# Kernel tuning notes

Measured on AMD Instinct MI355X. Metric: run time of the kernel, lower is better.

The kernel has to match this reference:

```python
import jax, jax.numpy as jnp
import numpy as np
from jax import lax

B, N, C = 128, 197, 384      # batch, tokens (1 cls + 14*14), embed dim
H, HD = 6, 64                # num_heads, head_dim
HID = 1536                   # mlp hidden = 4*C
S = 14                       # spatial side, S*S = N-1
SCALE = HD ** -0.5


def setup_inputs() -> dict:
    key = jax.random.key(0)
    ks = jax.random.split(key, 12)
    rn = lambda k, shp, s=0.02: jax.random.normal(k, shp, jnp.float32) * s
    return {
        "x": jax.random.normal(ks[0], (B, N, C), jnp.float32),
        "ln1_g": jnp.ones((C,), jnp.float32), "ln1_b": jnp.zeros((C,), jnp.float32),
        "qkv_w": rn(ks[1], (C, 3 * C)), "qkv_b": jnp.zeros((3 * C,), jnp.float32),
        "proj_w": rn(ks[2], (C, C)), "proj_b": jnp.zeros((C,), jnp.float32),
        "ht_w": rn(ks[3], (HD, C)), "ht_b": jnp.zeros((C,), jnp.float32),
        "htn_g": jnp.ones((HD,), jnp.float32), "htn_b": jnp.zeros((HD,), jnp.float32),
        "pos_embed": rn(ks[4], (1, H, C)),
        "ln2_g": jnp.ones((C,), jnp.float32), "ln2_b": jnp.zeros((C,), jnp.float32),
        "c1_w": rn(ks[5], (C, HID)), "c1_b": jnp.zeros((HID,), jnp.float32),
        "bn1_g": jnp.ones((HID,), jnp.float32), "bn1_b": jnp.zeros((HID,), jnp.float32),
        "c2_w": rn(ks[6], (HID, 1, 3, 3)), "c2_b": jnp.zeros((HID,), jnp.float32),
        "bn2_g": jnp.ones((HID,), jnp.float32), "bn2_b": jnp.zeros((HID,), jnp.float32),
        "c3_w": rn(ks[7], (HID, C)), "c3_b": jnp.zeros((C,), jnp.float32),
        "bn3_g": jnp.ones((C,), jnp.float32), "bn3_b": jnp.zeros((C,), jnp.float32),
        "cmp_w": rn(ks[8], (C, C // 4)), "cmp_b": jnp.zeros((C // 4,), jnp.float32),
        "exc_w": rn(ks[9], (C // 4, C)), "exc_b": jnp.zeros((C,), jnp.float32),
    }


def _ln(x, g, b, eps=1e-5):
    m = jnp.mean(x, -1, keepdims=True)
    v = jnp.var(x, -1, keepdims=True)
    return (x - m) * lax.rsqrt(v + eps) * g + b


def _gelu(x):
    return jax.nn.gelu(x, approximate=False)  # torch nn.GELU default = exact erf


def _bn(x, g, b, eps=1e-5):
    # eval-mode BatchNorm2d with running_mean=0, running_var=1; x is NCHW
    s = (g * lax.rsqrt(jnp.float32(1.0 + eps)))[None, :, None, None]
    return x * s + b[None, :, None, None]


def reference(x, ln1_g, ln1_b, qkv_w, qkv_b, proj_w, proj_b, ht_w, ht_b, htn_g, htn_b, pos_embed, ln2_g, ln2_b, c1_w, c1_b, bn1_g, bn1_b, c2_w, c2_b, bn2_g, bn2_b, c3_w, c3_b, bn3_g, bn3_b, cmp_w, cmp_b, exc_w, exc_b):
    # ---------- HI attention branch ----------
    xn = _ln(x, ln1_g, ln1_b)
    # per-head token mean: reshape [B,N,H,hd] -> mean over tokens -> [B,H,hd]
    xh = jnp.mean(xn.reshape(B, N, H, HD), axis=1)
    xh = xh @ ht_w + ht_b                                       # ht_proj: [B,H,C]
    xh = _gelu(_ln(xh.reshape(B, H, H, HD), htn_g, htn_b)).reshape(B, H, C)
    xh = xh + pos_embed                                          # head pos embed
    xa = jnp.concatenate([xn, xh], axis=1)                       # [B,M,C], M=N+H
    M = N + H
    qkv = (xa @ qkv_w + qkv_b).reshape(B, M, 3, H, HD)
    q, k, v = [jnp.transpose(qkv[:, :, i], (0, 2, 1, 3)) for i in range(3)]  # [B,H,M,hd]
    attn = jax.nn.softmax(jnp.einsum("bhqd,bhkd->bhqk", q, k) * SCALE, axis=-1)
    out = jnp.einsum("bhqk,bhkd->bhqd", attn, v)
    out = jnp.transpose(out, (0, 2, 1, 3)).reshape(B, M, C) @ proj_w + proj_b
    cls = out[:, :1] + jnp.mean(out[:, N:], axis=1, keepdims=True)  # cls += mean of head-tokens
    x1 = x + jnp.concatenate([cls, out[:, 1:N]], axis=1)
    # ---------- DAFF branch ----------
    xn2 = _ln(x1, ln2_g, ln2_b)
    cls2 = xn2[:, :1]
    t = jnp.transpose(xn2[:, 1:].reshape(B, S, S, C), (0, 3, 1, 2))  # NCHW
    h = _gelu(_bn(jnp.einsum("bchw,cd->bdhw", t, c1_w) + c1_b[None, :, None, None], bn1_g, bn1_b))
    dw = lax.conv_general_dilated(h, c2_w, (1, 1), "SAME", feature_group_count=HID,
                                  dimension_numbers=("NCHW", "OIHW", "NCHW"))
    h = h + _gelu(_bn(dw + c2_b[None, :, None, None], bn2_g, bn2_b))
    y = _bn(jnp.einsum("bchw,cd->bdhw", h, c3_w) + c3_b[None, :, None, None], bn3_g, bn3_b)
    w = jnp.mean(y, axis=(2, 3)).reshape(B, 1, C)                # squeeze
    w = _gelu(w @ cmp_w + cmp_b) @ exc_w + exc_b                 # compress -> excitation
    tok = jnp.transpose(y.reshape(B, C, S * S), (0, 2, 1))
    return x1 + jnp.concatenate([cls2 * w, tok], axis=1)
```

## Files before the change

### kernel.cpp

```cpp
#include <hip/hip_runtime.h>
#include <math.h>
#include <stdint.h>

#define B_   128
#define N_   197
#define C_   384
#define H_   6
#define HD_  64
#define HID_ 1536
#define S_   14
#define M_   203
#define P_   196
#define TC_  1152

typedef __bf16 bf16_t;
typedef __bf16 bf16x8 __attribute__((ext_vector_type(8)));
typedef float  f32x4  __attribute__((ext_vector_type(4)));

static constexpr size_t R1_OFF   = 0;
static constexpr size_t R2_OFF   = 119734272;
static constexpr size_t R3_OFF   = 159645696;
static constexpr size_t X1_OFF   = 179601408;
static constexpr size_t WQ_OFF   = 218333184;
static constexpr size_t WP_OFF   = 219217920;
static constexpr size_t W1_OFF   = 219512832;
static constexpr size_t W3_OFF   = 220692480;
static constexpr size_t CLS2_OFF = 221872128;
static constexpr size_t WSE_OFF  = 222461952;
static constexpr size_t WS_BYTES = 222658560;

__device__ __forceinline__ float gelu_f(float x) {
    return 0.5f * x * (1.0f + erff(x * 0.70710678118654752440f));
}
__device__ __forceinline__ float wave_sum(float v) {
    #pragma unroll
    for (int o = 32; o > 0; o >>= 1) v += __shfl_xor(v, o);
    return v;
}
__device__ __forceinline__ void gl_lds16(const void* g, void* l) {
    __builtin_amdgcn_global_load_lds(
        (const __attribute__((address_space(1))) uint32_t*)g,
        (__attribute__((address_space(3))) uint32_t*)l, 16, 0, 0);
}
__device__ __forceinline__ uint32_t pkbf(float a, float b) {
    uint16_t ua = __builtin_bit_cast(uint16_t, (bf16_t)a);
    uint16_t ub = __builtin_bit_cast(uint16_t, (bf16_t)b);
    return (uint32_t)ua | ((uint32_t)ub << 16);
}

__global__ __launch_bounds__(256) void k_wT(const float* __restrict__ W, bf16_t* __restrict__ Wt,
                                            int K, int N)
{
    __shared__ float t[32][33];
    int kb = blockIdx.x * 32, nb = blockIdx.y * 32;
    int tx = threadIdx.x & 31, ty = threadIdx.x >> 5;
    #pragma unroll
    for (int i = 0; i < 4; ++i)
        t[ty + i*8][tx] = W[(size_t)(kb + ty + i*8) * N + nb + tx];
    __syncthreads();
    #pragma unroll
    for (int i = 0; i < 4; ++i)
        Wt[(size_t)(nb + ty + i*8) * K + kb + tx] = (bf16_t)t[tx][ty + i*8];
}

__global__ __launch_bounds__(256) void k_ln1(const float* __restrict__ x,
        const float* __restrict__ g, const float* __restrict__ bt, bf16_t* __restrict__ xa)
{
    int row = blockIdx.x * 4 + (threadIdx.x >> 6);
    if (row >= B_ * N_) return;
    int lane = threadIdx.x & 63;
    int b = row / N_, n = row % N_;
    const float* xr = x + (size_t)row * C_;
    float v[6], s = 0.f, sq = 0.f;
    #pragma unroll
    for (int i = 0; i < 6; ++i) { v[i] = xr[lane + 64*i]; s += v[i]; sq += v[i]*v[i]; }
    s = wave_sum(s); sq = wave_sum(sq);
    float mean = s * (1.0f / C_);
    float var  = sq * (1.0f / C_) - mean * mean;
    float rstd = rsqrtf(var + 1e-5f);
    bf16_t* orow = xa + ((size_t)b * M_ + n) * C_;
    #pragma unroll
    for (int i = 0; i < 6; ++i) {
        int c = lane + 64*i;
        orow[c] = (bf16_t)((v[i] - mean) * rstd * g[c] + bt[c]);
    }
}

__global__ __launch_bounds__(384) void k_head_tokens(const bf16_t* __restrict__ xa_in,
    const float* __restrict__ ht_w, const float* __restrict__ ht_b,
    const float* __restrict__ htn_g, const float* __restrict__ htn_b,
    const float* __restrict__ pos, bf16_t* __restrict__ xa)
{
    __shared__ float hs[C_];
    int b = blockIdx.x, c = threadIdx.x, lane = c & 63;
    float s = 0.f;
    for (int n = 0; n < N_; ++n) s += (float)xa_in[((size_t)b * M_ + n) * C_ + c];
    hs[c] = s * (1.0f / N_);
    __syncthreads();
    for (int h1 = 0; h1 < H_; ++h1) {
        float acc = ht_b[c];
        #pragma unroll 8
        for (int d = 0; d < HD_; ++d) acc += hs[h1*HD_ + d] * ht_w[d*C_ + c];
        float mean = wave_sum(acc) * (1.0f / HD_);
        float sq   = wave_sum(acc*acc) * (1.0f / HD_);
        float var  = sq - mean*mean;
        float nv = (acc - mean) * rsqrtf(var + 1e-5f) * htn_g[lane] + htn_b[lane];
        xa[((size_t)b*M_ + N_ + h1)*C_ + c] = (bf16_t)(gelu_f(nv) + pos[h1*C_ + c]);
    }
}

template<int EPI>
__global__ __launch_bounds__(256) void k_mgemm(
    const bf16_t* __restrict__ A, const bf16_t* __restrict__ Bt,
    float* __restrict__ Cf, bf16_t* __restrict__ Cb,
    const float* __restrict__ bias, const float* __restrict__ bng,
    const float* __restrict__ bnb, int K, int Nc)
{
    __shared__ __align__(16) bf16_t As[128*32];
    __shared__ __align__(16) bf16_t Bs[128*32];
    int tid = threadIdx.x;
    int wave = tid >> 6, lane = tid & 63;
    int wm = wave >> 1, wn = wave & 1;
    int m_base = blockIdx.y * 128, n_base = blockIdx.x * 128;

    int sr = tid >> 2, ss = tid & 3;
    int sk8 = ss ^ ((sr >> 1) & 3);
    const bf16_t* gA = A  + (size_t)(m_base + sr) * K + sk8 * 8;
    const bf16_t* gB = Bt + (size_t)(n_base + sr) * K + sk8 * 8;
    char* AsB = (char*)As; char* BsB = (char*)Bs;

    int lr = lane & 15, lk = lane >> 4;
    int slot = lk ^ ((lr >> 1) & 3);
    int a_off = wm*4096 + lr*64 + slot*16;
    int b_off = wn*4096 + lr*64 + slot*16;

    f32x4 acc[4][4];
    #pragma unroll
    for (int i = 0; i < 4; ++i)
        #pragma unroll
        for (int j = 0; j < 4; ++j) acc[i][j] = (f32x4){0.f,0.f,0.f,0.f};

    for (int k0 = 0; k0 < K; k0 += 32) {
        gl_lds16(gA + k0,                 AsB + tid*16);
        gl_lds16(gA + k0 + (size_t)64*K,  AsB + 4096 + tid*16);
        gl_lds16(gB + k0,                 BsB + tid*16);
        gl_lds16(gB + k0 + (size_t)64*K,  BsB + 4096 + tid*16);
        __syncthreads();
        bf16x8 af[4], bfr[4];
        #pragma unroll
        for (int i = 0; i < 4; ++i) {
            af[i]  = *(const bf16x8*)(AsB + a_off + i*1024);
            bfr[i] = *(const bf16x8*)(BsB + b_off + i*1024);
        }
        #pragma unroll
        for (int i = 0; i < 4; ++i)
            #pragma unroll
            for (int j = 0; j < 4; ++j)
                acc[i][j] = __builtin_amdgcn_mfma_f32_16x16x32_bf16(af[i], bfr[j], acc[i][j], 0, 0, 0);
        __syncthreads();
    }

    const float R_ = 0.99999500003749969f;
    #pragma unroll
    for (int nf = 0; nf < 4; ++nf) {
        int n = n_base + wn*64 + nf*16 + lr;
        float bia = bias[n];
        float sc = 1.f, sh = 0.f;
        if (EPI == 1 || EPI == 2) { sc = bng[n] * R_; sh = bnb[n]; }
        #pragma unroll
        for (int mf = 0; mf < 4; ++mf) {
            size_t mrow = (size_t)m_base + wm*64 + mf*16 + lk*4;
            #pragma unroll
            for (int j = 0; j < 4; ++j) {
                float v = acc[mf][nf][j] + bia;
                if (EPI == 1 || EPI == 2) v = v * sc + sh;
                if (EPI == 1) v = gelu_f(v);
                if (EPI == 1 || EPI == 3) Cb[(mrow + j) * Nc + n] = (bf16_t)v;
                else                      Cf[(mrow + j) * Nc + n] = v;
            }
        }
    }
}

__global__ __launch_bounds__(512) void k_attn_mfma(const bf16_t* __restrict__ qkv,
                                                   bf16_t* __restrict__ aout)
{
    __shared__ __align__(16) bf16_t Ks[224*64];
    __shared__ __align__(16) bf16_t Vt[64][232];
    int b = blockIdx.x / H_, h = blockIdx.x % H_;
    const bf16_t* qb = qkv + (size_t)b * M_ * TC_ + h * HD_;
    const bf16_t* kb = qb + C_;
    const bf16_t* vb = qb + 2 * C_;
    int tid = threadIdx.x;

    #pragma unroll
    for (int it = 0; it < 4; ++it) {
        int idx = tid + it * 512;
        if (idx < 1792) {
            int r = idx >> 3, s = idx & 7;
            int sg = s ^ (r & 7);
            gl_lds16(kb + (size_t)r * TC_ + sg * 8, ((char*)Ks) + idx * 16);
        }
    }
    {
        int d0 = (tid & 31) * 2;
        uint16_t* vt0 = (uint16_t*)&Vt[d0][0];
        uint16_t* vt1 = (uint16_t*)&Vt[d0 + 1][0];
        for (int k = tid >> 5; k < 224; k += 16) {
            uint32_t u = 0;
            if (k < M_) u = *(const uint32_t*)(vb + (size_t)k * TC_ + d0);
            vt0[k] = (uint16_t)(u & 0xffff);
            vt1[k] = (uint16_t)(u >> 16);
        }
    }
    __syncthreads();

    int lane = tid & 63, wave = tid >> 6;
    int q16 = lane & 15, g = lane >> 4;
    int base4g = g * 4;
    int s0 = q16 + (g & 1) * 32, s1 = s0 + 16;
    bool sel = (lane >= 32);

    for (int qt = wave; qt < 13; qt += 8) {
        int qrow = qt * 16 + q16;
        bf16x8 qf0 = *(const bf16x8*)(qb + (size_t)qrow * TC_ + g * 8);
        bf16x8 qf1 = *(const bf16x8*)(qb + (size_t)qrow * TC_ + 32 + g * 8);

        f32x4 sacc[14];
        #pragma unroll
        for (int t = 0; t < 14; ++t) sacc[t] = (f32x4){0.f, 0.f, 0.f, 0.f};
        #pragma unroll
        for (int kt = 0; kt < 14; ++kt) {
            int r = kt * 16 + q16;
            const char* rowp = (const char*)Ks + r * 128;
            bf16x8 kf0 = *(const bf16x8*)(rowp + ((g ^ (r & 7)) * 16));
            bf16x8 kf1 = *(const bf16x8*)(rowp + (((4 + g) ^ (r & 7)) * 16));
            sacc[kt] = __builtin_amdgcn_mfma_f32_16x16x32_bf16(kf0, qf0, sacc[kt], 0, 0, 0);
            sacc[kt] = __builtin_amdgcn_mfma_f32_16x16x32_bf16(kf1, qf1, sacc[kt], 0, 0, 0);
        }

        float mx = -1e30f;
        #pragma unroll
        for (int t = 0; t < 14; ++t)
            #pragma unroll
            for (int j = 0; j < 4; ++j) {
                int key = 16 * t + base4g + j;
                float v = (key < M_) ? sacc[t][j] * 0.125f : -1e30f;
                sacc[t][j] = v;
                mx = fmaxf(mx, v);
            }
        mx = fmaxf(mx, __shfl_xor(mx, 16));
        mx = fmaxf(mx, __shfl_xor(mx, 32));
        float sm = 0.f;
        #pragma unroll
        for (int t = 0; t < 14; ++t)
            #pragma unroll
            for (int j = 0; j < 4; ++j) {
                float e = __expf(sacc[t][j] - mx);
                sacc[t][j] = e;
                sm += e;
            }
        sm += __shfl_xor(sm, 16);
        sm += __shfl_xor(sm, 32);
        float inv = 1.0f / sm;

        uint32_t plo[14], phi[14];
        #pragma unroll
        for (int t = 0; t < 14; ++t) {
            plo[t] = pkbf(sacc[t][0] * inv, sacc[t][1] * inv);
            phi[t] = pkbf(sacc[t][2] * inv, sacc[t][3] * inv);
        }

        f32x4 oacc[4];
        #pragma unroll
        for (int dt = 0; dt < 4; ++dt) oacc[dt] = (f32x4){0.f, 0.f, 0.f, 0.f};
        #pragma unroll
        for (int c = 0; c < 7; ++c) {
            uint32_t l0a = (uint32_t)__shfl((int)plo[2*c],     s0);
            uint32_t l1a = (uint32_t)__shfl((int)plo[2*c + 1], s0);
            uint32_t h0a = (uint32_t)__shfl((int)phi[2*c],     s0);
            uint32_t h1a = (uint32_t)__shfl((int)phi[2*c + 1], s0);
            uint32_t l0b = (uint32_t)__shfl((int)plo[2*c],     s1);
            uint32_t l1b = (uint32_t)__shfl((int)plo[2*c + 1], s1);
            uint32_t h0b = (uint32_t)__shfl((int)phi[2*c],     s1);
            uint32_t h1b = (uint32_t)__shfl((int)phi[2*c + 1], s1);
            union { uint32_t u[4]; bf16x8 v; } pf;
            pf.u[0] = sel ? l1a : l0a;
            pf.u[1] = sel ? h1a : h0a;
            pf.u[2] = sel ? l1b : l0b;
            pf.u[3] = sel ? h1b : h0b;
            #pragma unroll
            for (int dt = 0; dt < 4; ++dt) {
                bf16x8 vf = *(const bf16x8*)(&Vt[dt*16 + q16][c*32 + g*8]);
                oacc[dt] = __builtin_amdgcn_mfma_f32_16x16x32_bf16(pf.v, vf, oacc[dt], 0, 0, 0);
            }
        }

        #pragma unroll
        for (int dt = 0; dt < 4; ++dt)
            #pragma unroll
            for (int j = 0; j < 4; ++j) {
                int q = qt * 16 + base4g + j;
                if (q < M_)
                    aout[((size_t)b * M_ + q) * C_ + h * HD_ + dt * 16 + q16] = (bf16_t)oacc[dt][j];
            }
    }
}

__global__ __launch_bounds__(256) void k_x1ln2(const float* __restrict__ x,
    const float* __restrict__ proj, const float* __restrict__ g, const float* __restrict__ bt,
    float* __restrict__ x1, bf16_t* __restrict__ xn2, float* __restrict__ cls2)
{
    int row = blockIdx.x * 4 + (threadIdx.x >> 6);
    if (row >= B_ * N_) return;
    int lane = threadIdx.x & 63;
    int b = row / N_, n = row % N_;
    const float* xr = x + (size_t)row * C_;
    const float* pr = proj + (size_t)b * M_ * C_;
    float v[6], s = 0.f, sq = 0.f;
    #pragma unroll
    for (int i = 0; i < 6; ++i) {
        int c = lane + 64*i;
        float t;
        if (n == 0) {
            float m = 0.f;
            #pragma unroll
            for (int mm = 0; mm < H_; ++mm) m += pr[(size_t)(N_ + mm) * C_ + c];
            t = xr[c] + pr[c] + m * (1.0f / H_);
        } else {
            t = xr[c] + pr[(size_t)n * C_ + c];
        }
        v[i] = t; s += t; sq += t*t;
    }
    float* x1r = x1 + (size_t)row * C_;
    #pragma unroll
    for (int i = 0; i < 6; ++i) x1r[lane + 64*i] = v[i];
    s = wave_sum(s); sq = wave_sum(sq);
    float mean = s * (1.0f / C_);
    float var  = sq * (1.0f / C_) - mean * mean;
    float rstd = rsqrtf(var + 1e-5f);
    #pragma unroll
    for (int i = 0; i < 6; ++i) {
        int c = lane + 64*i;
        float ov = (v[i] - mean) * rstd * g[c] + bt[c];
        if (n == 0) cls2[(size_t)b * C_ + c] = ov;
        else        xn2[((size_t)b * P_ + (n - 1)) * C_ + c] = (bf16_t)ov;
    }
}

__global__ __launch_bounds__(256) void k_dwconv(bf16_t* __restrict__ h,
    const float* __restrict__ w, const float* __restrict__ c2b,
    const float* __restrict__ g2, const float* __restrict__ b2)
{
    __shared__ float tile[P_][64];
    __shared__ float wl[64][9];
    int b = blockIdx.x, ch0 = blockIdx.y * 64;
    for (int idx = threadIdx.x; idx < P_ * 64; idx += 256) {
        int p = idx >> 6, c = idx & 63;
        tile[p][c] = (float)h[((size_t)b * P_ + p) * HID_ + ch0 + c];
    }
    if (threadIdx.x < 64) {
        int c = threadIdx.x;
        #pragma unroll
        for (int k = 0; k < 9; ++k) wl[c][k] = w[(ch0 + c) * 9 + k];
    }
    __syncthreads();
    const float R_ = 0.99999500003749969f;
    for (int idx = threadIdx.x; idx < P_ * 64; idx += 256) {
        int p = idx >> 6, c = idx & 63;
        int y = p / S_, xq = p % S_;
        float a = 0.f;
        #pragma unroll
        for (int dy = 0; dy < 3; ++dy) {
            int yy = y + dy - 1;
            if (yy < 0 || yy >= S_) continue;
            #pragma unroll
            for (int dx = 0; dx < 3; ++dx) {
                int xx = xq + dx - 1;
                if (xx < 0 || xx >= S_) continue;
                a += wl[c][dy*3+dx] * tile[yy*S_ + xx][c];
            }
        }
        int ch = ch0 + c;
        float val = (a + c2b[ch]) * (g2[ch] * R_) + b2[ch];
        h[((size_t)b * P_ + p) * HID_ + ch] = (bf16_t)(tile[p][c] + gelu_f(val));
    }
}

__global__ __launch_bounds__(384) void k_se(const float* __restrict__ y,
    const float* __restrict__ cw, const float* __restrict__ cb,
    const float* __restrict__ ew, const float* __restrict__ eb, float* __restrict__ wse)
{
    __shared__ float ys[C_];
    __shared__ float hid[96];
    int b = blockIdx.x, t = threadIdx.x;
    float s = 0.f;
    for (int p = 0; p < P_; ++p) s += y[((size_t)b * P_ + p) * C_ + t];
    ys[t] = s * (1.0f / P_);
    __syncthreads();
    if (t < 96) {
        float a = cb[t];
        for (int c = 0; c < C_; ++c) a += ys[c] * cw[c * 96 + t];
        hid[t] = gelu_f(a);
    }
    __syncthreads();
    float a = eb[t];
    #pragma unroll 8
    for (int j = 0; j < 96; ++j) a += hid[j] * ew[j * C_ + t];
    wse[b * C_ + t] = a;
}

__global__ void k_final(const float* __restrict__ x1, const float* __restrict__ y,
    const float* __restrict__ cls2, const float* __restrict__ wse, float* __restrict__ out)
{
    size_t idx = (size_t)blockIdx.x * 256 + threadIdx.x;
    if (idx >= (size_t)B_*N_*C_) return;
    int c = (int)(idx % C_);
    size_t t = idx / C_;
    int n = (int)(t % N_); int b = (int)(t / N_);
    float v = x1[idx];
    if (n == 0) v += cls2[b*C_ + c] * wse[b*C_ + c];
    else        v += y[((size_t)b * P_ + (n - 1)) * C_ + c];
    out[idx] = v;
}

extern "C" void kernel_launch(void* const* d_in, const int* in_sizes, int n_in,
                              void* d_out, int out_size, void* d_ws, size_t ws_size,
                              hipStream_t stream)
{
    const float* x      = (const float*)d_in[0];
    const float* ln1_g  = (const float*)d_in[1];
    const float* ln1_b  = (const float*)d_in[2];
    const float* qkv_w  = (const float*)d_in[3];
    const float* qkv_b  = (const float*)d_in[4];
    const float* proj_w = (const float*)d_in[5];
    const float* proj_b = (const float*)d_in[6];
    const float* ht_w   = (const float*)d_in[7];
    const float* ht_b   = (const float*)d_in[8];
    const float* htn_g  = (const float*)d_in[9];
    const float* htn_b  = (const float*)d_in[10];
    const float* pos    = (const float*)d_in[11];
    const float* ln2_g  = (const float*)d_in[12];
    const float* ln2_b  = (const float*)d_in[13];
    const float* c1_w   = (const float*)d_in[14];
    const float* c1_b   = (const float*)d_in[15];
    const float* bn1_g  = (const float*)d_in[16];
    const float* bn1_b  = (const float*)d_in[17];
    const float* c2_w   = (const float*)d_in[18];
    const float* c2_b   = (const float*)d_in[19];
    const float* bn2_g  = (const float*)d_in[20];
    const float* bn2_b  = (const float*)d_in[21];
    const float* c3_w   = (const float*)d_in[22];
    const float* c3_b   = (const float*)d_in[23];
    const float* bn3_g  = (const float*)d_in[24];
    const float* bn3_b  = (const float*)d_in[25];
    const float* cmp_w  = (const float*)d_in[26];
    const float* cmp_b  = (const float*)d_in[27];
    const float* exc_w  = (const float*)d_in[28];
    const float* exc_b  = (const float*)d_in[29];

    if (ws_size < WS_BYTES) return;
    char* ws = (char*)d_ws;
    bf16_t* QKVb = (bf16_t*)(ws + R1_OFF);
    bf16_t* HBUF = (bf16_t*)(ws + R1_OFF);
    float*  PROJ = (float*)(ws + R2_OFF);
    bf16_t* XN2  = (bf16_t*)(ws + R2_OFF);
    float*  Y    = (float*)(ws + R2_OFF);
    bf16_t* XA   = (bf16_t*)(ws + R3_OFF);
    bf16_t* AOUT = (bf16_t*)(ws + R3_OFF);
    float*  X1   = (float*)(ws + X1_OFF);
    bf16_t* WQT  = (bf16_t*)(ws + WQ_OFF);
    bf16_t* WPT  = (bf16_t*)(ws + WP_OFF);
    bf16_t* W1T  = (bf16_t*)(ws + W1_OFF);
    bf16_t* W3T  = (bf16_t*)(ws + W3_OFF);
    float*  CLS2 = (float*)(ws + CLS2_OFF);
    float*  WSE  = (float*)(ws + WSE_OFF);

    k_wT<<<dim3(C_/32,  TC_/32), 256, 0, stream>>>(qkv_w,  WQT, C_,  TC_);
    k_wT<<<dim3(C_/32,  C_/32),  256, 0, stream>>>(proj_w, WPT, C_,  C_);
    k_wT<<<dim3(C_/32,  HID_/32),256, 0, stream>>>(c1_w,   W1T, C_,  HID_);
    k_wT<<<dim3(HID_/32,C_/32),  256, 0, stream>>>(c3_w,   W3T, HID_, C_);

    k_ln1<<<(B_*N_ + 3) / 4, 256, 0, stream>>>(x, ln1_g, ln1_b, XA);
    k_head_tokens<<<B_, 384, 0, stream>>>(XA, ht_w, ht_b, htn_g, htn_b, pos, XA);

    k_mgemm<3><<<dim3(TC_/128, (B_*M_)/128), 256, 0, stream>>>(
        XA, WQT, nullptr, QKVb, qkv_b, nullptr, nullptr, C_, TC_);

    k_attn_mfma<<<B_*H_, 512, 0, stream>>>(QKVb, AOUT);

    k_mgemm<0><<<dim3(C_/128, (B_*M_)/128), 256, 0, stream>>>(
        AOUT, WPT, PROJ, nullptr, proj_b, nullptr, nullptr, C_, C_);

    k_x1ln2<<<(B_*N_ + 3) / 4, 256, 0, stream>>>(x, PROJ, ln2_g, ln2_b, X1, XN2, CLS2);

    k_mgemm<1><<<dim3(HID_/128, (B_*P_)/128), 256, 0, stream>>>(
        XN2, W1T, nullptr, HBUF, c1_b, bn1_g, bn1_b, C_, HID_);

    k_dwconv<<<dim3(B_, HID_/64), 256, 0, stream>>>(HBUF, c2_w, c2_b, bn2_g, bn2_b);

    k_mgemm<2><<<dim3(C_/128, (B_*P_)/128), 256, 0, stream>>>(
        HBUF, W3T, Y, nullptr, c3_b, bn3_g, bn3_b, HID_, C_);

    k_se<<<B_, 384, 0, stream>>>(Y, cmp_w, cmp_b, exc_w, exc_b, WSE);
    k_final<<<(B_*N_*C_ + 255)/256, 256, 0, stream>>>(X1, Y, CLS2, WSE, (float*)d_out);
}
```

Measured before the change: 665.5 us.

## Rewrite depthwise conv as per-row register kernel with separate output buffer

Replaces the LDS-tiled in-place depthwise 3x3 conv with a kernel where each thread handles one channel for one image row, loading three input rows into registers and writing to a separate output buffer. This removes the shared-memory tile, the barrier and the per-element index division, and launches many more blocks (B*14 by 6) for better occupancy. Out-of-place output requires reshuffling the workspace layout and increases the workspace size. Each input row is now read three times from global memory, relying on cache for reuse, and register pressure rises from the 42-value row buffer.

```diff
diff --git a/kernel.cpp b/kernel.cpp
--- a/kernel.cpp
+++ b/kernel.cpp
@@ -17,17 +17,17 @@
 typedef __bf16 bf16x8 __attribute__((ext_vector_type(8)));
 typedef float  f32x4  __attribute__((ext_vector_type(4)));
 
-static constexpr size_t R1_OFF   = 0;
-static constexpr size_t R2_OFF   = 119734272;
-static constexpr size_t R3_OFF   = 159645696;
-static constexpr size_t X1_OFF   = 179601408;
-static constexpr size_t WQ_OFF   = 218333184;
-static constexpr size_t WP_OFF   = 219217920;
-static constexpr size_t W1_OFF   = 219512832;
-static constexpr size_t W3_OFF   = 220692480;
-static constexpr size_t CLS2_OFF = 221872128;
-static constexpr size_t WSE_OFF  = 222461952;
-static constexpr size_t WS_BYTES = 222658560;
+static constexpr size_t OFF_A    = 0;
+static constexpr size_t OFF_B    = 77070336;
+static constexpr size_t OFF_P    = 154140672;
+static constexpr size_t OFF_X1   = 194052096;
+static constexpr size_t OFF_WQ   = 232783872;
+static constexpr size_t OFF_WP   = 233668608;
+static constexpr size_t OFF_W1   = 233963520;
+static constexpr size_t OFF_W3   = 235143168;
+static constexpr size_t OFF_CLS2 = 236322816;
+static constexpr size_t OFF_WSE  = 236519424;
+static constexpr size_t WS_BYTES = 236716032;
 
 __device__ __forceinline__ float gelu_f(float x) {
     return 0.5f * x * (1.0f + erff(x * 0.70710678118654752440f));
@@ -348,42 +348,44 @@
     }
 }
 
-__global__ __launch_bounds__(256) void k_dwconv(bf16_t* __restrict__ h,
-    const float* __restrict__ w, const float* __restrict__ c2b,
+__global__ __launch_bounds__(256) void k_dwconv2(const bf16_t* __restrict__ hin,
+    bf16_t* __restrict__ hout, const float* __restrict__ w, const float* __restrict__ c2b,
     const float* __restrict__ g2, const float* __restrict__ b2)
 {
-    __shared__ float tile[P_][64];
-    __shared__ float wl[64][9];
-    int b = blockIdx.x, ch0 = blockIdx.y * 64;
-    for (int idx = threadIdx.x; idx < P_ * 64; idx += 256) {
-        int p = idx >> 6, c = idx & 63;
-        tile[p][c] = (float)h[((size_t)b * P_ + p) * HID_ + ch0 + c];
-    }
-    if (threadIdx.x < 64) {
-        int c = threadIdx.x;
-        #pragma unroll
-        for (int k = 0; k < 9; ++k) wl[c][k] = w[(ch0 + c) * 9 + k];
-    }
-    __syncthreads();
+    int by = blockIdx.x;
+    int b = by / S_, y = by % S_;
+    int ch = blockIdx.y * 256 + threadIdx.x;
+    const bf16_t* base = hin + (size_t)b * P_ * HID_ + ch;
+
+    float v[3][14];
+    #pragma unroll
+    for (int dy = 0; dy < 3; ++dy) {
+        int yy = y + dy - 1;
+        bool ok = (yy >= 0) && (yy < S_);
+        #pragma unroll
+        for (int xx = 0; xx < S_; ++xx)
+            v[dy][xx] = ok ? (float)base[(size_t)(yy * S_ + xx) * HID_] : 0.f;
+    }
+    float wl[9];
+    #pragma unroll
+    for (int k = 0; k < 9; ++k) wl[k] = w[ch * 9 + k];
     const float R_ = 0.99999500003749969f;
-    for (int idx = threadIdx.x; idx < P_ * 64; idx += 256) {
-        int p = idx >> 6, c = idx & 63;
-        int y = p / S_, xq = p % S_;
+    float bc = c2b[ch], gg = g2[ch] * R_, bb = b2[ch];
+
+    bf16_t* obase = hout + ((size_t)b * P_ + y * S_) * HID_ + ch;
+    #pragma unroll
+    for (int x = 0; x < S_; ++x) {
         float a = 0.f;
         #pragma unroll
-        for (int dy = 0; dy < 3; ++dy) {
-            int yy = y + dy - 1;
-            if (yy < 0 || yy >= S_) continue;
+        for (int dy = 0; dy < 3; ++dy)
             #pragma unroll
             for (int dx = 0; dx < 3; ++dx) {
-                int xx = xq + dx - 1;
+                int xx = x + dx - 1;
                 if (xx < 0 || xx >= S_) continue;
-                a += wl[c][dy*3+dx] * tile[yy*S_ + xx][c];
+                a += wl[dy*3 + dx] * v[dy][xx];
             }
-        }
-        int ch = ch0 + c;
-        float val = (a + c2b[ch]) * (g2[ch] * R_) + b2[ch];
-        h[((size_t)b * P_ + p) * HID_ + ch] = (bf16_t)(tile[p][c] + gelu_f(val));
+        float val = (a + bc) * gg + bb;
+        obase[(size_t)x * HID_] = (bf16_t)(v[1][x] + gelu_f(val));
     }
 }
 
@@ -461,20 +463,21 @@
 
     if (ws_size < WS_BYTES) return;
     char* ws = (char*)d_ws;
-    bf16_t* QKVb = (bf16_t*)(ws + R1_OFF);
-    bf16_t* HBUF = (bf16_t*)(ws + R1_OFF);
-    float*  PROJ = (float*)(ws + R2_OFF);
-    bf16_t* XN2  = (bf16_t*)(ws + R2_OFF);
-    float*  Y    = (float*)(ws + R2_OFF);
-    bf16_t* XA   = (bf16_t*)(ws + R3_OFF);
-    bf16_t* AOUT = (bf16_t*)(ws + R3_OFF);
-    float*  X1   = (float*)(ws + X1_OFF);
-    bf16_t* WQT  = (bf16_t*)(ws + WQ_OFF);
-    bf16_t* WPT  = (bf16_t*)(ws + WP_OFF);
-    bf16_t* W1T  = (bf16_t*)(ws + W1_OFF);
-    bf16_t* W3T  = (bf16_t*)(ws + W3_OFF);
-    float*  CLS2 = (float*)(ws + CLS2_OFF);
-    float*  WSE  = (float*)(ws + WSE_OFF);
+    bf16_t* QKVb  = (bf16_t*)(ws + OFF_A);
+    bf16_t* HBUFA = (bf16_t*)(ws + OFF_A);
+    bf16_t* XA    = (bf16_t*)(ws + OFF_B);
+    bf16_t* AOUT  = (bf16_t*)(ws + OFF_B);
+    bf16_t* XN2   = (bf16_t*)(ws + OFF_B);
+    bf16_t* HBUFB = (bf16_t*)(ws + OFF_B);
+    float*  PROJ  = (float*)(ws + OFF_P);
+    float*  Y     = (float*)(ws + OFF_P);
+    float*  X1    = (float*)(ws + OFF_X1);
+    bf16_t* WQT   = (bf16_t*)(ws + OFF_WQ);
+    bf16_t* WPT   = (bf16_t*)(ws + OFF_WP);
+    bf16_t* W1T   = (bf16_t*)(ws + OFF_W1);
+    bf16_t* W3T   = (bf16_t*)(ws + OFF_W3);
+    float*  CLS2  = (float*)(ws + OFF_CLS2);
+    float*  WSE   = (float*)(ws + OFF_WSE);
 
     k_wT<<<dim3(C_/32,  TC_/32), 256, 0, stream>>>(qkv_w,  WQT, C_,  TC_);
     k_wT<<<dim3(C_/32,  C_/32),  256, 0, stream>>>(proj_w, WPT, C_,  C_);
@@ -495,12 +498,12 @@
     k_x1ln2<<<(B_*N_ + 3) / 4, 256, 0, stream>>>(x, PROJ, ln2_g, ln2_b, X1, XN2, CLS2);
 
     k_mgemm<1><<<dim3(HID_/128, (B_*P_)/128), 256, 0, stream>>>(
-        XN2, W1T, nullptr, HBUF, c1_b, bn1_g, bn1_b, C_, HID_);
-
-    k_dwconv<<<dim3(B_, HID_/64), 256, 0, stream>>>(HBUF, c2_w, c2_b, bn2_g, bn2_b);
+        XN2, W1T, nullptr, HBUFA, c1_b, bn1_g, bn1_b, C_, HID_);
+
+    k_dwconv2<<<dim3(B_*S_, HID_/256), 256, 0, stream>>>(HBUFA, HBUFB, c2_w, c2_b, bn2_g, bn2_b);
 
     k_mgemm<2><<<dim3(C_/128, (B_*P_)/128), 256, 0, stream>>>(
-        HBUF, W3T, Y, nullptr, c3_b, bn3_g, bn3_b, HID_, C_);
+        HBUFB, W3T, Y, nullptr, c3_b, bn3_g, bn3_b, HID_, C_);
 
     k_se<<<B_, 384, 0, stream>>>(Y, cmp_w, cmp_b, exc_w, exc_b, WSE);
     k_final<<<(B_*N_*C_ + 255)/256, 256, 0, stream>>>(X1, Y, CLS2, WSE, (float*)d_out);
```

After: 668.3 us. No clear change (+0.4%).
